# Kernel optimization log

Measured on AMD Instinct MI355X. Metric: run time of the kernel, lower is better.

The kernel has to match this reference:

```python
import jax, jax.numpy as jnp
import numpy as np

T, B, D, L, A, H = 64, 256, 512, 50, 18, 32


def setup_inputs() -> dict:
    key = jax.random.key(0)
    ks = jax.random.split(key, 12)
    s = 0.05
    return {
        "state": jax.random.normal(ks[0], (T, B, D), jnp.float32),
        "demonstration": jax.random.normal(ks[1], (T, B, L, D), jnp.float32),
        "h0": jnp.zeros((1, B, H), jnp.float32),
        "c0": jnp.zeros((1, B, H), jnp.float32),
        # attn: Linear(H + D, L)
        "W_attn": jax.random.normal(ks[2], (L, H + D), jnp.float32) * s,
        "b_attn": jnp.zeros((L,), jnp.float32),
        # attn_combine: Linear(2*D, H)
        "W_comb": jax.random.normal(ks[3], (H, 2 * D), jnp.float32) * s,
        "b_comb": jnp.zeros((H,), jnp.float32),
        # LSTM(H, H): gate order i, f, g, o
        "W_ih": jax.random.normal(ks[4], (4 * H, H), jnp.float32) * s,
        "b_ih": jnp.zeros((4 * H,), jnp.float32),
        "W_hh": jax.random.normal(ks[5], (4 * H, H), jnp.float32) * s,
        "b_hh": jnp.zeros((4 * H,), jnp.float32),
        # middle: Linear(H, 2H); output: Linear(2H, A)
        "W_mid": jax.random.normal(ks[6], (2 * H, H), jnp.float32) * s,
        "b_mid": jnp.zeros((2 * H,), jnp.float32),
        "W_out": jax.random.normal(ks[7], (A, 2 * H), jnp.float32) * s,
        "b_out": jnp.zeros((A,), jnp.float32),
    }


def reference(state, demonstration, h0, c0, W_attn, b_attn, W_comb, b_comb,
              W_ih, b_ih, W_hh, b_hh, W_mid, b_mid, W_out, b_out):
    def step(carry, inp):
        h, c = carry                         # [B,H], [B,H]
        cur, demo = inp                      # [B,D], [B,L,D]
        logits = jnp.concatenate([cur, h], axis=-1) @ W_attn.T + b_attn  # [B,L]
        w = jax.nn.softmax(logits, axis=1)
        applied = jnp.einsum('bl,bld->bd', w, demo)                      # [B,D]
        x = jax.nn.relu(jnp.concatenate([applied, cur], axis=-1) @ W_comb.T + b_comb)  # [B,H]
        gates = x @ W_ih.T + b_ih + h @ W_hh.T + b_hh                    # [B,4H]
        i, f, g, o = jnp.split(gates, 4, axis=-1)
        c_new = jax.nn.sigmoid(f) * c + jax.nn.sigmoid(i) * jnp.tanh(g)
        h_new = jax.nn.sigmoid(o) * jnp.tanh(c_new)
        mid = h_new @ W_mid.T + b_mid                                    # [B,2H]
        q = mid @ W_out.T + b_out                                        # [B,A]
        return (h_new, c_new), q

    (hT, cT), q = jax.lax.scan(step, (h0[0], c0[0]), (state, demonstration))
    return q, hT[None], cT[None]
```

## Files before the change

### kernel.cpp

```cpp
#include <hip/hip_runtime.h>
#include <cstddef>

#define T_ 64
#define B_ 256
#define D_ 512
#define L_ 50
#define A_ 18
#define H_ 32

typedef __attribute__((ext_vector_type(8))) short short8;
typedef __attribute__((ext_vector_type(4))) float f32x4;

constexpr size_t WS_LC   = 0;
constexpr size_t WS_CC   = 819200;
constexpr size_t WS_WQ   = 1343488;
constexpr size_t WS_BQ   = 1344064;
constexpr size_t WS_HIST = 1344128;
constexpr size_t WS_DP   = 1868416;

__device__ __forceinline__ float sigf(float x) { return 1.f / (1.f + expf(-x)); }

__device__ __forceinline__ short f2bf_rne(float f) {
  unsigned u = __float_as_uint(f);
  return (short)((u + 0x7fffu + ((u >> 16) & 1u)) >> 16);
}
__device__ __forceinline__ float bcast(float v, int l) {
  return __int_as_float(__builtin_amdgcn_readlane(__float_as_int(v), l));
}
__device__ __forceinline__ void glds16(const float* g, float* l) {
  __builtin_amdgcn_global_load_lds((const __attribute__((address_space(1))) unsigned*)g,
                                   (__attribute__((address_space(3))) unsigned*)l, 16, 0, 0);
}
__device__ __forceinline__ void glds4(const float* g, float* l) {
  __builtin_amdgcn_global_load_lds((const __attribute__((address_space(1))) unsigned*)g,
                                   (__attribute__((address_space(3))) unsigned*)l, 4, 0, 0);
}

__global__ __launch_bounds__(512) void precompute2(
    const float* __restrict__ state,
    const float* __restrict__ W_attn, const float* __restrict__ b_attn,
    const float* __restrict__ W_comb, const float* __restrict__ b_comb,
    float* __restrict__ lc, float* __restrict__ cc) {
  __shared__ float scur[24 * 512];
  const int tid = threadIdx.x;
  const int r0 = blockIdx.x * 24;
  for (int f = tid; f < 24 * 512; f += 512) {
    int r = r0 + (f >> 9);
    scur[f] = (r < 16384) ? state[(size_t)r * 512 + (f & 511)] : 0.f;
  }
  __syncthreads();
  if (tid >= 492) return;
  const int j = tid % 82, rg = tid / 82;
  const float* wrow = (j < 50) ? (W_attn + (size_t)j * 544)
                               : (W_comb + (size_t)(j - 50) * 1024 + 512);
  const float bias = (j < 50) ? b_attn[j] : b_comb[j - 50];
  const f32x4* w4 = (const f32x4*)wrow;
  const f32x4* s4 = (const f32x4*)scur;
  float acc[4] = {0.f, 0.f, 0.f, 0.f};
#pragma unroll 2
  for (int k4 = 0; k4 < 128; ++k4) {
    f32x4 w = w4[k4];
#pragma unroll
    for (int rr = 0; rr < 4; ++rr) {
      f32x4 s = s4[(rg * 4 + rr) * 128 + k4];
      acc[rr] = fmaf(s.x, w.x, acc[rr]);
      acc[rr] = fmaf(s.y, w.y, acc[rr]);
      acc[rr] = fmaf(s.z, w.z, acc[rr]);
      acc[rr] = fmaf(s.w, w.w, acc[rr]);
    }
  }
#pragma unroll
  for (int rr = 0; rr < 4; ++rr) {
    int r = r0 + rg * 4 + rr;
    if (r < 16384) {
      if (j < 50) lc[(size_t)r * 50 + j] = acc[rr] + bias;
      else        cc[(size_t)r * 32 + (j - 50)] = acc[rr] + bias;
    }
  }
}

__global__ __launch_bounds__(576) void wq_fold(
    const float* __restrict__ W_mid, const float* __restrict__ b_mid,
    const float* __restrict__ W_out, const float* __restrict__ b_out,
    float* __restrict__ wqt, float* __restrict__ bq) {
  const int tid = threadIdx.x;
  if (tid < 576) {
    const int a = tid / 32, k = tid % 32;
    float acc = 0.f;
#pragma unroll
    for (int m = 0; m < 64; ++m) acc = fmaf(W_out[a * 64 + m], W_mid[m * 32 + k], acc);
    wqt[k * 18 + a] = acc;
  }
  if (tid < 18) {
    float acc = b_out[tid];
#pragma unroll
    for (int m = 0; m < 64; ++m) acc = fmaf(W_out[tid * 64 + m], b_mid[m], acc);
    bq[tid] = acc;
  }
}

__global__ __launch_bounds__(512, 2) void dp_gemm(const float* __restrict__ demo,
                                                  const float* __restrict__ W_comb,
                                                  float* __restrict__ dp) {
  extern __shared__ char smraw[];
  float* Abuf = (float*)smraw;
  short* frag = (short*)(smraw + 65536);
  const int tid = threadIdx.x;

  for (int f = tid; f < 16384; f += 512) {
    int j = f & 7, l = (f >> 3) & 63, nt = (f >> 9) & 1, c = f >> 10;
    int n = nt * 16 + (l & 15);
    int k = c * 32 + ((l >> 4) << 3) + j;
    float v = W_comb[(size_t)n * 1024 + k];
    unsigned u = __float_as_uint(v);
    unsigned hb = u & 0xffff0000u;
    frag[(((0 * 16 + c) * 2 + nt) * 64 + l) * 8 + j] = (short)(hb >> 16);
    frag[(((1 * 16 + c) * 2 + nt) * 64 + l) * 8 + j] = f2bf_rne(v - __uint_as_float(hb));
  }
  __syncthreads();

  const int wave = tid >> 6, lane = tid & 63;
  const size_t row0 = (size_t)blockIdx.x * 3200;

  int rrl[4], gcol[4];
#pragma unroll
  for (int i = 0; i < 4; ++i) {
    rrl[i] = wave * 16 + i * 4 + (lane >> 4);
    gcol[i] = ((((lane & 15) * 16) ^ ((rrl[i] & 7) << 4)) >> 2);
  }

  const int rr = wave * 16 + (lane & 15);
  const int g = lane >> 4;

  f32x4 acc0 = {0.f, 0.f, 0.f, 0.f}, acc1 = {0.f, 0.f, 0.f, 0.f};

#define STAGE(Q, SLOT)                                                          \
  {                                                                             \
    const int tile_ = (Q) >> 3, kc_ = (Q) & 7;                                  \
    const size_t rbase_ = row0 + (size_t)tile_ * 128;                           \
    float* dst_ = Abuf + (SLOT) * 8192 + wave * 1024;                           \
    _Pragma("unroll")                                                           \
    for (int i = 0; i < 4; ++i) {                                               \
      const float* src_ = demo + (rbase_ + rrl[i]) * 512 + kc_ * 64 + gcol[i];  \
      glds16(src_, dst_ + i * 256);                                             \
    }                                                                           \
  }

  STAGE(0, 0);
  for (int q = 0; q < 200; ++q) {
    const int qn = (q + 1 < 200) ? q + 1 : 199;
    STAGE(qn, (q + 1) & 1);
    asm volatile("s_waitcnt vmcnt(4)" ::: "memory");
    __builtin_amdgcn_sched_barrier(0);
    if ((q & 7) == 0) {
      acc0 = {0.f, 0.f, 0.f, 0.f};
      acc1 = {0.f, 0.f, 0.f, 0.f};
    }
    const char* ab = (const char*)(Abuf + (q & 1) * 8192) + rr * 256;
#pragma unroll
    for (int sub = 0; sub < 2; ++sub) {
      const int b0 = (sub * 128 + g * 32) ^ ((rr & 7) << 4);
      f32x4 a0 = *(const f32x4*)(ab + b0);
      f32x4 a1 = *(const f32x4*)(ab + (b0 ^ 16));
      short8 ahi, alo;
#pragma unroll
      for (int j = 0; j < 4; ++j) {
        float v = a0[j];
        unsigned u = __float_as_uint(v), hb = u & 0xffff0000u;
        ahi[j] = (short)(hb >> 16);
        alo[j] = f2bf_rne(v - __uint_as_float(hb));
        float w = a1[j];
        unsigned u2 = __float_as_uint(w), hb2 = u2 & 0xffff0000u;
        ahi[4 + j] = (short)(hb2 >> 16);
        alo[4 + j] = f2bf_rne(w - __uint_as_float(hb2));
      }
      const int ck = (q & 7) * 2 + sub;
      short8 bh0 = *(const short8*)&frag[(((0 + ck) * 2 + 0) * 64 + lane) * 8];
      short8 bh1 = *(const short8*)&frag[(((0 + ck) * 2 + 1) * 64 + lane) * 8];
      short8 bl0 = *(const short8*)&frag[(((16 + ck) * 2 + 0) * 64 + lane) * 8];
      short8 bl1 = *(const short8*)&frag[(((16 + ck) * 2 + 1) * 64 + lane) * 8];
      acc0 = __builtin_amdgcn_mfma_f32_16x16x32_bf16(ahi, bh0, acc0, 0, 0, 0);
      acc1 = __builtin_amdgcn_mfma_f32_16x16x32_bf16(ahi, bh1, acc1, 0, 0, 0);
      acc0 = __builtin_amdgcn_mfma_f32_16x16x32_bf16(alo, bh0, acc0, 0, 0, 0);
      acc1 = __builtin_amdgcn_mfma_f32_16x16x32_bf16(alo, bh1, acc1, 0, 0, 0);
      acc0 = __builtin_amdgcn_mfma_f32_16x16x32_bf16(ahi, bl0, acc0, 0, 0, 0);
      acc1 = __builtin_amdgcn_mfma_f32_16x16x32_bf16(ahi, bl1, acc1, 0, 0, 0);
    }
    if ((q & 7) == 7) {
      float* drow = dp + (row0 + (size_t)(q >> 3) * 128 + wave * 16) * 32;
#pragma unroll
      for (int reg = 0; reg < 4; ++reg) {
        int r = ((lane >> 4) << 2) + reg;
        drow[r * 32 + (lane & 15)] = acc0[reg];
        drow[r * 32 + 16 + (lane & 15)] = acc1[reg];
      }
    }
  }
#undef STAGE
}

__global__ __launch_bounds__(64, 1) void seq2(
    const float* __restrict__ h0, const float* __restrict__ c0,
    const float* __restrict__ W_attn,
    const float* __restrict__ W_ih, const float* __restrict__ b_ih,
    const float* __restrict__ W_hh, const float* __restrict__ b_hh,
    const float* __restrict__ ws, float* __restrict__ histg,
    float* __restrict__ out) {
  __shared__ alignas(16) float dpb[3][1600];
  __shared__ alignas(16) float lcb[3][64];
  __shared__ alignas(16) float ccb[3][64];
  __shared__ alignas(16) float hist[T_ * 32];
  const int b = blockIdx.x, lane = threadIdx.x, hh = lane & 31;
  const float* lcg = ws + WS_LC;
  const float* ccg = ws + WS_CC;
  const float* dpg = ws + WS_DP;

  float wA2[32], wia[32], wib[32], wha[32], whb[32];
  const int l_eff = lane < 50 ? lane : 49;
#pragma unroll
  for (int k = 0; k < 32; ++k) {
    wA2[k] = W_attn[(size_t)l_eff * 544 + 512 + k];
    wia[k] = W_ih[lane * 32 + k];
    wib[k] = W_ih[(64 + lane) * 32 + k];
    wha[k] = W_hh[lane * 32 + k];
    whb[k] = W_hh[(64 + lane) * 32 + k];
  }
  const float bga = b_ih[lane] + b_hh[lane];
  const float bgb = b_ih[64 + lane] + b_hh[64 + lane];
  float h = h0[b * 32 + hh], c = c0[b * 32 + hh];

#pragma unroll
  for (int tt = 0; tt < 2; ++tt) {
    const size_t rown = (size_t)tt * B_ + b;
    const float* dsrc = dpg + rown * 1600;
#pragma unroll
    for (int i = 0; i < 6; ++i) glds16(dsrc + i * 256 + lane * 4, &dpb[tt][i * 256]);
    glds4(dsrc + 1536 + lane, &dpb[tt][1536]);
    glds4(lcg + rown * 50 + lane, &lcb[tt][0]);
    glds4(ccg + rown * 32 + lane, &ccb[tt][0]);
  }

  int p = 0;
  for (int t = 0; t < T_; ++t) {
    const int pn = (p >= 1) ? p - 1 : p + 2;
    {
      const size_t rown = (size_t)(t + 2) * B_ + b;
      const float* dsrc = dpg + rown * 1600;
#pragma unroll
      for (int i = 0; i < 6; ++i) glds16(dsrc + i * 256 + lane * 4, &dpb[pn][i * 256]);
      glds4(dsrc + 1536 + lane, &dpb[pn][1536]);
      glds4(lcg + rown * 50 + lane, &lcb[pn][0]);
      glds4(ccg + rown * 32 + lane, &ccb[pn][0]);
    }
    asm volatile("s_waitcnt vmcnt(18)" ::: "memory");
    __builtin_amdgcn_sched_barrier(0);

    float lg0 = 0.f, lg1 = 0.f;
#pragma unroll
    for (int k = 0; k < 32; k += 2) {
      lg0 = fmaf(bcast(h, k), wA2[k], lg0);
      lg1 = fmaf(bcast(h, k + 1), wA2[k + 1], lg1);
    }
    const float logit = (lane < 50) ? (lcb[p][lane] + lg0 + lg1) : -1e30f;
    float mx = logit;
#pragma unroll
    for (int off = 32; off; off >>= 1) mx = fmaxf(mx, __shfl_xor(mx, off, 64));
    const float e = (lane < 50) ? expf(logit - mx) : 0.f;
    float se = e;
#pragma unroll
    for (int off = 32; off; off >>= 1) se += __shfl_xor(se, off, 64);
    const float wsm = e / se;

    float xl0 = 0.f, xl1 = 0.f;
#pragma unroll
    for (int l = 0; l < 50; l += 2) {
      xl0 = fmaf(bcast(wsm, l), dpb[p][l * 32 + hh], xl0);
      xl1 = fmaf(bcast(wsm, l + 1), dpb[p][(l + 1) * 32 + hh], xl1);
    }
    const float x = fmaxf(xl0 + xl1 + ccb[p][hh], 0.f);

    float ga0 = bga, ga1 = 0.f, gb0 = bgb, gb1 = 0.f;
#pragma unroll
    for (int k = 0; k < 32; k += 2) {
      float xv0 = bcast(x, k), hv0 = bcast(h, k);
      float xv1 = bcast(x, k + 1), hv1 = bcast(h, k + 1);
      ga0 = fmaf(xv0, wia[k], ga0);     ga0 = fmaf(hv0, wha[k], ga0);
      ga1 = fmaf(xv1, wia[k + 1], ga1); ga1 = fmaf(hv1, wha[k + 1], ga1);
      gb0 = fmaf(xv0, wib[k], gb0);     gb0 = fmaf(hv0, whb[k], gb0);
      gb1 = fmaf(xv1, wib[k + 1], gb1); gb1 = fmaf(hv1, whb[k + 1], gb1);
    }
    const float ga = ga0 + ga1, gb = gb0 + gb1;
    const float xga = __shfl_xor(ga, 32, 64), xgb = __shfl_xor(gb, 32, 64);
    const bool low = lane < 32;
    const float iv = low ? ga : xga, fv = low ? xga : ga;
    const float gv = low ? gb : xgb, ov = low ? xgb : gb;
    c = sigf(fv) * c + sigf(iv) * tanhf(gv);
    h = sigf(ov) * tanhf(c);
    if (lane < 32) hist[t * 32 + hh] = h;

    p = (p + 1 == 3) ? 0 : p + 1;
  }

  for (int f = lane; f < 512; f += 64)
    ((f32x4*)(histg + (size_t)b * 2048))[f] = ((const f32x4*)hist)[f];
  if (lane < 32) {
    out[(size_t)T_ * B_ * A_ + (size_t)b * H_ + lane] = h;
    out[(size_t)T_ * B_ * A_ + (size_t)B_ * H_ + (size_t)b * H_ + lane] = c;
  }
}

__global__ __launch_bounds__(256) void q_kernel(
    const float* __restrict__ histg, const float* __restrict__ wqt,
    const float* __restrict__ bq, float* __restrict__ out) {
  __shared__ float sh[64 * 33];
  __shared__ float swq[576];
  __shared__ float sbq[18];
  const int b = blockIdx.x, tid = threadIdx.x;
  for (int f = tid; f < 2048; f += 256) {
    int t = f >> 5, k = f & 31;
    sh[t * 33 + k] = histg[(size_t)b * 2048 + f];
  }
  for (int f = tid; f < 576; f += 256) swq[f] = wqt[f];
  if (tid < 18) sbq[tid] = bq[tid];
  __syncthreads();
  for (int idx = tid; idx < 1152; idx += 256) {
    int t = idx / 18, a = idx - t * 18;
    float acc = sbq[a];
#pragma unroll
    for (int k = 0; k < 32; ++k) acc = fmaf(sh[t * 33 + k], swq[k * 18 + a], acc);
    out[((size_t)t * B_ + b) * A_ + a] = acc;
  }
}

extern "C" void kernel_launch(void* const* d_in, const int* in_sizes, int n_in,
                              void* d_out, int out_size, void* d_ws, size_t ws_size,
                              hipStream_t stream) {
  const float* state  = (const float*)d_in[0];
  const float* demo   = (const float*)d_in[1];
  const float* h0     = (const float*)d_in[2];
  const float* c0     = (const float*)d_in[3];
  const float* W_attn = (const float*)d_in[4];
  const float* b_attn = (const float*)d_in[5];
  const float* W_comb = (const float*)d_in[6];
  const float* b_comb = (const float*)d_in[7];
  const float* W_ih   = (const float*)d_in[8];
  const float* b_ih   = (const float*)d_in[9];
  const float* W_hh   = (const float*)d_in[10];
  const float* b_hh   = (const float*)d_in[11];
  const float* W_mid  = (const float*)d_in[12];
  const float* b_mid  = (const float*)d_in[13];
  const float* W_out  = (const float*)d_in[14];
  const float* b_out  = (const float*)d_in[15];
  float* out = (float*)d_out;
  float* ws  = (float*)d_ws;

  wq_fold<<<dim3(1), dim3(576), 0, stream>>>(
      W_mid, b_mid, W_out, b_out, ws + WS_WQ, ws + WS_BQ);
  precompute2<<<dim3(683), dim3(512), 0, stream>>>(
      state, W_attn, b_attn, W_comb, b_comb, ws + WS_LC, ws + WS_CC);

  constexpr int dp_smem = 131072;
  (void)hipFuncSetAttribute(reinterpret_cast<const void*>(dp_gemm),
                            hipFuncAttributeMaxDynamicSharedMemorySize, dp_smem);
  dp_gemm<<<dim3(256), dim3(512), dp_smem, stream>>>(demo, W_comb, ws + WS_DP);

  seq2<<<dim3(256), dim3(64), 0, stream>>>(
      h0, c0, W_attn, W_ih, b_ih, W_hh, b_hh, ws, ws + WS_HIST, out);
  q_kernel<<<dim3(256), dim3(256), 0, stream>>>(
      ws + WS_HIST, ws + WS_WQ, ws + WS_BQ, out);
}
```

Measured before the change: 609.9 us.

## Use MFMA for state projection, triple-buffer dp_gemm, fuse Q head into sequence kernel

Replaces the scalar-FMA state projection with an MFMA-based split-bf16 GEMM (hi/lo emulation of fp32) over 64-row tiles. dp_gemm moves from double to triple buffering with a deeper prefetch distance and more LDS. The wq fold and Q output projection are folded into the sequential LSTM kernel, which removes two launches and the history round trip through global memory. The trade-offs are extra serial work at the end of the latency-bound recurrence, lower dp_gemm occupancy from the larger LDS footprint, and slightly different rounding from the bf16 split.

```diff
diff --git a/kernel.cpp b/kernel.cpp
--- a/kernel.cpp
+++ b/kernel.cpp
@@ -11,12 +11,9 @@
 typedef __attribute__((ext_vector_type(8))) short short8;
 typedef __attribute__((ext_vector_type(4))) float f32x4;
 
-constexpr size_t WS_LC   = 0;
-constexpr size_t WS_CC   = 819200;
-constexpr size_t WS_WQ   = 1343488;
-constexpr size_t WS_BQ   = 1344064;
-constexpr size_t WS_HIST = 1344128;
-constexpr size_t WS_DP   = 1868416;
+constexpr size_t WS_LC = 0;
+constexpr size_t WS_CC = 819200;
+constexpr size_t WS_DP = 1868416;
 
 __device__ __forceinline__ float sigf(float x) { return 1.f / (1.f + expf(-x)); }
 
@@ -36,66 +33,130 @@
                                    (__attribute__((address_space(3))) unsigned*)l, 4, 0, 0);
 }
 
-__global__ __launch_bounds__(512) void precompute2(
+__global__ __launch_bounds__(256) void precompute3(
     const float* __restrict__ state,
     const float* __restrict__ W_attn, const float* __restrict__ b_attn,
     const float* __restrict__ W_comb, const float* __restrict__ b_comb,
     float* __restrict__ lc, float* __restrict__ cc) {
-  __shared__ float scur[24 * 512];
+  extern __shared__ char pm3[];
+  float* As = (float*)pm3;
+  short* Bf = (short*)(pm3 + 16384);
   const int tid = threadIdx.x;
-  const int r0 = blockIdx.x * 24;
-  for (int f = tid; f < 24 * 512; f += 512) {
-    int r = r0 + (f >> 9);
-    scur[f] = (r < 16384) ? state[(size_t)r * 512 + (f & 511)] : 0.f;
-  }
-  __syncthreads();
-  if (tid >= 492) return;
-  const int j = tid % 82, rg = tid / 82;
-  const float* wrow = (j < 50) ? (W_attn + (size_t)j * 544)
-                               : (W_comb + (size_t)(j - 50) * 1024 + 512);
-  const float bias = (j < 50) ? b_attn[j] : b_comb[j - 50];
-  const f32x4* w4 = (const f32x4*)wrow;
-  const f32x4* s4 = (const f32x4*)scur;
-  float acc[4] = {0.f, 0.f, 0.f, 0.f};
-#pragma unroll 2
-  for (int k4 = 0; k4 < 128; ++k4) {
-    f32x4 w = w4[k4];
-#pragma unroll
-    for (int rr = 0; rr < 4; ++rr) {
-      f32x4 s = s4[(rg * 4 + rr) * 128 + k4];
-      acc[rr] = fmaf(s.x, w.x, acc[rr]);
-      acc[rr] = fmaf(s.y, w.y, acc[rr]);
-      acc[rr] = fmaf(s.z, w.z, acc[rr]);
-      acc[rr] = fmaf(s.w, w.w, acc[rr]);
-    }
-  }
-#pragma unroll
-  for (int rr = 0; rr < 4; ++rr) {
-    int r = r0 + rg * 4 + rr;
-    if (r < 16384) {
-      if (j < 50) lc[(size_t)r * 50 + j] = acc[rr] + bias;
-      else        cc[(size_t)r * 32 + (j - 50)] = acc[rr] + bias;
-    }
-  }
-}
-
-__global__ __launch_bounds__(576) void wq_fold(
-    const float* __restrict__ W_mid, const float* __restrict__ b_mid,
-    const float* __restrict__ W_out, const float* __restrict__ b_out,
-    float* __restrict__ wqt, float* __restrict__ bq) {
-  const int tid = threadIdx.x;
-  if (tid < 576) {
-    const int a = tid / 32, k = tid % 32;
-    float acc = 0.f;
-#pragma unroll
-    for (int m = 0; m < 64; ++m) acc = fmaf(W_out[a * 64 + m], W_mid[m * 32 + k], acc);
-    wqt[k * 18 + a] = acc;
-  }
-  if (tid < 18) {
-    float acc = b_out[tid];
-#pragma unroll
-    for (int m = 0; m < 64; ++m) acc = fmaf(W_out[tid * 64 + m], b_mid[m], acc);
-    bq[tid] = acc;
+  const int wave = tid >> 6, lane = tid & 63;
+  const int r0 = blockIdx.x * 64;
+
+  const int srow = lane >> 3;
+  const int scol = (((lane & 7) * 16) ^ (srow << 4)) >> 2;
+  const int crow = lane & 15, g = lane >> 4;
+  const int cb0 = (g * 32) ^ ((crow & 7) << 4);
+
+  f32x4 acc[6];
+#pragma unroll
+  for (int nt = 0; nt < 6; ++nt) acc[nt] = {0.f, 0.f, 0.f, 0.f};
+
+#define STAGE_A(KI, SLOT)                                                       \
+  {                                                                             \
+    float* dst_ = As + ((SLOT) * 4 + wave) * 512;                               \
+    _Pragma("unroll")                                                           \
+    for (int i_ = 0; i_ < 2; ++i_) {                                            \
+      const float* src_ = state +                                               \
+          (size_t)(r0 + wave * 16 + i_ * 8 + srow) * 512 + (KI) * 32 + scol;    \
+      glds16(src_, dst_ + i_ * 256);                                            \
+    }                                                                           \
+  }
+
+  auto stageB = [&](int ko) {
+#pragma unroll
+    for (int it = 0; it < 6; ++it) {
+      int u = tid + it * 256;
+      int l = u & 63;
+      int nt = (u >> 6) % 6;
+      int c = u / 384;
+      int n = nt * 16 + (l & 15);
+      int kb = ko * 128 + c * 32 + ((l >> 4) << 3);
+      f32x4 v0 = {0.f, 0.f, 0.f, 0.f}, v1 = {0.f, 0.f, 0.f, 0.f};
+      if (n < 50) {
+        const f32x4* s = (const f32x4*)(W_attn + (size_t)n * 544 + kb);
+        v0 = s[0]; v1 = s[1];
+      } else if (n < 82) {
+        const f32x4* s = (const f32x4*)(W_comb + (size_t)(n - 50) * 1024 + 512 + kb);
+        v0 = s[0]; v1 = s[1];
+      }
+      short8 hi, lo;
+#pragma unroll
+      for (int j = 0; j < 4; ++j) {
+        unsigned ua = __float_as_uint(v0[j]), ha = ua & 0xffff0000u;
+        hi[j] = (short)(ha >> 16);
+        lo[j] = f2bf_rne(v0[j] - __uint_as_float(ha));
+        unsigned ub = __float_as_uint(v1[j]), hb = ub & 0xffff0000u;
+        hi[4 + j] = (short)(hb >> 16);
+        lo[4 + j] = f2bf_rne(v1[j] - __uint_as_float(hb));
+      }
+      *(short8*)&Bf[(((0 * 4 + c) * 6 + nt) * 64 + l) * 8] = hi;
+      *(short8*)&Bf[(((1 * 4 + c) * 6 + nt) * 64 + l) * 8] = lo;
+    }
+  };
+
+  STAGE_A(0, 0);
+  stageB(0);
+  asm volatile("s_waitcnt lgkmcnt(0)" ::: "memory");
+  __builtin_amdgcn_s_barrier();
+
+  for (int ko = 0; ko < 4; ++ko) {
+    if (ko > 0) {
+      __builtin_amdgcn_s_barrier();
+      stageB(ko);
+      asm volatile("s_waitcnt lgkmcnt(0)" ::: "memory");
+      __builtin_amdgcn_s_barrier();
+    }
+#pragma unroll
+    for (int c = 0; c < 4; ++c) {
+      const int ki = ko * 4 + c;
+      if (ki < 15) {
+        STAGE_A(ki + 1, (ki + 1) & 1);
+        asm volatile("s_waitcnt vmcnt(2)" ::: "memory");
+      } else {
+        asm volatile("s_waitcnt vmcnt(0)" ::: "memory");
+      }
+      __builtin_amdgcn_sched_barrier(0);
+      const char* ab = (const char*)(As + ((ki & 1) * 4 + wave) * 512) + crow * 128;
+      f32x4 a0 = *(const f32x4*)(ab + cb0);
+      f32x4 a1 = *(const f32x4*)(ab + (cb0 ^ 16));
+      short8 ahi, alo;
+#pragma unroll
+      for (int j = 0; j < 4; ++j) {
+        unsigned ua = __float_as_uint(a0[j]), ha = ua & 0xffff0000u;
+        ahi[j] = (short)(ha >> 16);
+        alo[j] = f2bf_rne(a0[j] - __uint_as_float(ha));
+        unsigned ub = __float_as_uint(a1[j]), hb = ub & 0xffff0000u;
+        ahi[4 + j] = (short)(hb >> 16);
+        alo[4 + j] = f2bf_rne(a1[j] - __uint_as_float(hb));
+      }
+#pragma unroll
+      for (int nt = 0; nt < 6; ++nt) {
+        short8 bh = *(const short8*)&Bf[(((0 * 4 + c) * 6 + nt) * 64 + lane) * 8];
+        short8 bl = *(const short8*)&Bf[(((1 * 4 + c) * 6 + nt) * 64 + lane) * 8];
+        acc[nt] = __builtin_amdgcn_mfma_f32_16x16x32_bf16(ahi, bh, acc[nt], 0, 0, 0);
+        acc[nt] = __builtin_amdgcn_mfma_f32_16x16x32_bf16(alo, bh, acc[nt], 0, 0, 0);
+        acc[nt] = __builtin_amdgcn_mfma_f32_16x16x32_bf16(ahi, bl, acc[nt], 0, 0, 0);
+      }
+    }
+  }
+#undef STAGE_A
+
+#pragma unroll
+  for (int nt = 0; nt < 6; ++nt) {
+    const int n = nt * 16 + crow;
+    float bias = 0.f;
+    if (n < 50) bias = b_attn[n];
+    else if (n < 82) bias = b_comb[n - 50];
+#pragma unroll
+    for (int reg = 0; reg < 4; ++reg) {
+      const int r = r0 + wave * 16 + (g << 2) + reg;
+      const float vv = acc[nt][reg] + bias;
+      if (n < 50) lc[(size_t)r * 50 + n] = vv;
+      else if (n < 82) cc[(size_t)r * 32 + (n - 50)] = vv;
+    }
   }
 }
 
@@ -104,7 +165,7 @@
                                                   float* __restrict__ dp) {
   extern __shared__ char smraw[];
   float* Abuf = (float*)smraw;
-  short* frag = (short*)(smraw + 65536);
+  short* frag = (short*)(smraw + 98304);
   const int tid = threadIdx.x;
 
   for (int f = tid; f < 16384; f += 512) {
@@ -128,7 +189,6 @@
     rrl[i] = wave * 16 + i * 4 + (lane >> 4);
     gcol[i] = ((((lane & 15) * 16) ^ ((rrl[i] & 7) << 4)) >> 2);
   }
-
   const int rr = wave * 16 + (lane & 15);
   const int g = lane >> 4;
 
@@ -147,16 +207,21 @@
   }
 
   STAGE(0, 0);
+  STAGE(1, 1);
   for (int q = 0; q < 200; ++q) {
-    const int qn = (q + 1 < 200) ? q + 1 : 199;
-    STAGE(qn, (q + 1) & 1);
-    asm volatile("s_waitcnt vmcnt(4)" ::: "memory");
+    const int q2 = (q + 2 < 200) ? q + 2 : 199;
+    STAGE(q2, (q + 2) % 3);
+    if (q >= 8 && (q & 7) <= 1) {
+      asm volatile("s_waitcnt vmcnt(16)" ::: "memory");
+    } else {
+      asm volatile("s_waitcnt vmcnt(8)" ::: "memory");
+    }
     __builtin_amdgcn_sched_barrier(0);
     if ((q & 7) == 0) {
       acc0 = {0.f, 0.f, 0.f, 0.f};
       acc1 = {0.f, 0.f, 0.f, 0.f};
     }
-    const char* ab = (const char*)(Abuf + (q & 1) * 8192) + rr * 256;
+    const char* ab = (const char*)(Abuf + (q % 3) * 8192) + rr * 256;
 #pragma unroll
     for (int sub = 0; sub < 2; ++sub) {
       const int b0 = (sub * 128 + g * 32) ^ ((rr & 7) << 4);
@@ -199,17 +264,20 @@
 #undef STAGE
 }
 
-__global__ __launch_bounds__(64, 1) void seq2(
+__global__ __launch_bounds__(64, 1) void seq3(
     const float* __restrict__ h0, const float* __restrict__ c0,
     const float* __restrict__ W_attn,
     const float* __restrict__ W_ih, const float* __restrict__ b_ih,
     const float* __restrict__ W_hh, const float* __restrict__ b_hh,
-    const float* __restrict__ ws, float* __restrict__ histg,
-    float* __restrict__ out) {
+    const float* __restrict__ W_mid, const float* __restrict__ b_mid,
+    const float* __restrict__ W_out, const float* __restrict__ b_out,
+    const float* __restrict__ ws, float* __restrict__ out) {
   __shared__ alignas(16) float dpb[3][1600];
   __shared__ alignas(16) float lcb[3][64];
   __shared__ alignas(16) float ccb[3][64];
-  __shared__ alignas(16) float hist[T_ * 32];
+  __shared__ alignas(16) float hist[T_ * 33];
+  __shared__ float swq[576];
+  __shared__ float sbq[20];
   const int b = blockIdx.x, lane = threadIdx.x, hh = lane & 31;
   const float* lcg = ws + WS_LC;
   const float* ccg = ws + WS_CC;
@@ -238,6 +306,20 @@
     glds4(dsrc + 1536 + lane, &dpb[tt][1536]);
     glds4(lcg + rown * 50 + lane, &lcb[tt][0]);
     glds4(ccg + rown * 32 + lane, &ccb[tt][0]);
+  }
+
+  for (int idx = lane; idx < 576; idx += 64) {
+    int a = idx >> 5, k = idx & 31;
+    float acc = 0.f;
+#pragma unroll
+    for (int m = 0; m < 64; ++m) acc = fmaf(W_out[a * 64 + m], W_mid[m * 32 + k], acc);
+    swq[k * 18 + a] = acc;
+  }
+  if (lane < 18) {
+    float acc = b_out[lane];
+#pragma unroll
+    for (int m = 0; m < 64; ++m) acc = fmaf(W_out[lane * 64 + m], b_mid[m], acc);
+    sbq[lane] = acc;
   }
 
   int p = 0;
@@ -296,39 +378,21 @@
     const float gv = low ? gb : xgb, ov = low ? xgb : gb;
     c = sigf(fv) * c + sigf(iv) * tanhf(gv);
     h = sigf(ov) * tanhf(c);
-    if (lane < 32) hist[t * 32 + hh] = h;
+    if (lane < 32) hist[t * 33 + hh] = h;
 
     p = (p + 1 == 3) ? 0 : p + 1;
   }
 
-  for (int f = lane; f < 512; f += 64)
-    ((f32x4*)(histg + (size_t)b * 2048))[f] = ((const f32x4*)hist)[f];
+  for (int idx = lane; idx < T_ * A_; idx += 64) {
+    int t = idx / A_, a = idx - t * A_;
+    float acc = sbq[a];
+#pragma unroll
+    for (int k = 0; k < 32; ++k) acc = fmaf(hist[t * 33 + k], swq[k * 18 + a], acc);
+    out[((size_t)t * B_ + b) * A_ + a] = acc;
+  }
   if (lane < 32) {
     out[(size_t)T_ * B_ * A_ + (size_t)b * H_ + lane] = h;
     out[(size_t)T_ * B_ * A_ + (size_t)B_ * H_ + (size_t)b * H_ + lane] = c;
-  }
-}
-
-__global__ __launch_bounds__(256) void q_kernel(
-    const float* __restrict__ histg, const float* __restrict__ wqt,
-    const float* __restrict__ bq, float* __restrict__ out) {
-  __shared__ float sh[64 * 33];
-  __shared__ float swq[576];
-  __shared__ float sbq[18];
-  const int b = blockIdx.x, tid = threadIdx.x;
-  for (int f = tid; f < 2048; f += 256) {
-    int t = f >> 5, k = f & 31;
-    sh[t * 33 + k] = histg[(size_t)b * 2048 + f];
-  }
-  for (int f = tid; f < 576; f += 256) swq[f] = wqt[f];
-  if (tid < 18) sbq[tid] = bq[tid];
-  __syncthreads();
-  for (int idx = tid; idx < 1152; idx += 256) {
-    int t = idx / 18, a = idx - t * 18;
-    float acc = sbq[a];
-#pragma unroll
-    for (int k = 0; k < 32; ++k) acc = fmaf(sh[t * 33 + k], swq[k * 18 + a], acc);
-    out[((size_t)t * B_ + b) * A_ + a] = acc;
   }
 }
 
@@ -354,18 +418,18 @@
   float* out = (float*)d_out;
   float* ws  = (float*)d_ws;
 
-  wq_fold<<<dim3(1), dim3(576), 0, stream>>>(
-      W_mid, b_mid, W_out, b_out, ws + WS_WQ, ws + WS_BQ);
-  precompute2<<<dim3(683), dim3(512), 0, stream>>>(
+  constexpr int pm3_smem = 65536;
+  (void)hipFuncSetAttribute(reinterpret_cast<const void*>(precompute3),
+                            hipFuncAttributeMaxDynamicSharedMemorySize, pm3_smem);
+  precompute3<<<dim3(256), dim3(256), pm3_smem, stream>>>(
       state, W_attn, b_attn, W_comb, b_comb, ws + WS_LC, ws + WS_CC);
 
-  constexpr int dp_smem = 131072;
+  constexpr int dp_smem = 163840;
   (void)hipFuncSetAttribute(reinterpret_cast<const void*>(dp_gemm),
                             hipFuncAttributeMaxDynamicSharedMemorySize, dp_smem);
   dp_gemm<<<dim3(256), dim3(512), dp_smem, stream>>>(demo, W_comb, ws + WS_DP);
 
-  seq2<<<dim3(256), dim3(64), 0, stream>>>(
-      h0, c0, W_attn, W_ih, b_ih, W_hh, b_hh, ws, ws + WS_HIST, out);
-  q_kernel<<<dim3(256), dim3(256), 0, stream>>>(
-      ws + WS_HIST, ws + WS_WQ, ws + WS_BQ, out);
-}
+  seq3<<<dim3(256), dim3(64), 0, stream>>>(
+      h0, c0, W_attn, W_ih, b_ih, W_hh, b_hh,
+      W_mid, b_mid, W_out, b_out, ws, out);
+}
```

New measurement: 550.4 us. -9.8%, faster.
